# Kernel optimization log

Hardware: AMD Instinct MI355X
Metric: run time of the kernel (lower is better)

The kernel has to match this reference:

```python
import jax, jax.numpy as jnp
import numpy as np

B, L, E = 2, 8192, 1024
H, D = 16, 64          # num_heads, head_dim (E = H*D)
C = 256                # chunk_size
EPS = 1e-6
LN_EPS = 1e-5


def setup_inputs() -> dict:
    key = jax.random.key(0)
    ks = jax.random.split(key, 12)
    w = lambda k, shape: (jax.random.normal(k, shape, jnp.float32) * 0.02)
    return {
        "x": jax.random.normal(ks[0], (B, L, E), jnp.float32),
        "Wq": w(ks[1], (E, E)), "bq": jnp.zeros((E,), jnp.float32),
        "Wk": w(ks[2], (E, E)), "bk": jnp.zeros((E,), jnp.float32),
        "Wv": w(ks[3], (E, E)), "bv": jnp.zeros((E,), jnp.float32),
        "Wo": w(ks[4], (E, E)), "bo": jnp.zeros((E,), jnp.float32),
        "gamma": jnp.ones((E,), jnp.float32),
        "beta": jnp.zeros((E,), jnp.float32),
    }


def _split_heads(t):
    # [B, L, E] -> [B, H, L, D]
    return t.reshape(B, L, H, D).transpose(0, 2, 1, 3)


def _phi(x):
    # feature map: elu(x) + 1  (strictly positive)
    return jax.nn.elu(x) + 1.0


def _chunkwise_linear_attention(q, k, v):
    """Causal linear attention via chunkwise parallel scan.

    q, k, v: [B, H, L, D] (q, k already feature-mapped, positive).
    out[t] = q_t @ S_t / (q_t . z_t), S_t = sum_{s<=t} k_s v_s^T, z_t = sum_{s<=t} k_s.
    """
    N = L // C
    # [N, B, H, C, D]
    qc = q.reshape(B, H, N, C, D).transpose(2, 0, 1, 3, 4)
    kc = k.reshape(B, H, N, C, D).transpose(2, 0, 1, 3, 4)
    vc = v.reshape(B, H, N, C, D).transpose(2, 0, 1, 3, 4)
    mask = jnp.tril(jnp.ones((C, C), q.dtype))  # causal within chunk (inclusive)

    def step(carry, inp):
        S, z = carry                      # S: [B,H,D,D], z: [B,H,D]
        qi, ki, vi = inp                  # [B,H,C,D]
        scores = jnp.einsum("bhcd,bhed->bhce", qi, ki) * mask  # [B,H,C,C]
        num = jnp.einsum("bhcd,bhde->bhce", qi, S) \
            + jnp.einsum("bhce,bhed->bhcd", scores, vi)
        den = jnp.einsum("bhcd,bhd->bhc", qi, z) + scores.sum(-1)
        out = num / (den + EPS)[..., None]
        S = S + jnp.einsum("bhcd,bhce->bhde", ki, vi)
        z = z + ki.sum(axis=2)
        return (S, z), out

    S0 = jnp.zeros((B, H, D, D), q.dtype)
    z0 = jnp.zeros((B, H, D), q.dtype)
    _, outs = jax.lax.scan(step, (S0, z0), (qc, kc, vc))
    # [N,B,H,C,D] -> [B,H,L,D]
    return outs.transpose(1, 2, 0, 3, 4).reshape(B, H, L, D)


def _layer_norm(x, gamma, beta):
    mu = x.mean(-1, keepdims=True)
    var = ((x - mu) ** 2).mean(-1, keepdims=True)
    return gamma * (x - mu) * jax.lax.rsqrt(var + LN_EPS) + beta


def reference(x, Wq, bq, Wk, bk, Wv, bv, Wo, bo, gamma, beta):
    residual = x
    q = _phi(_split_heads(x @ Wq + bq))
    k = _phi(_split_heads(x @ Wk + bk))
    v = _split_heads(x @ Wv + bv)
    out = _chunkwise_linear_attention(q, k, v)      # [B,H,L,D]
    out = out.transpose(0, 2, 1, 3).reshape(B, L, E)
    out = out @ Wo + bo
    return _layer_norm(out + residual, gamma, beta)
```

## Files before the change

kernel.cpp:

```cpp
#include <hip/hip_runtime.h>
#include <stdint.h>

typedef __attribute__((ext_vector_type(8))) short bf16x8;
typedef __attribute__((ext_vector_type(4))) float f32x4;
typedef __attribute__((ext_vector_type(2))) unsigned int u32x2;
typedef unsigned short u16;
typedef unsigned int u32;

#define MFMA16(a, b, c) __builtin_amdgcn_mfma_f32_16x16x32_bf16((a), (b), (c), 0, 0, 0)
#define SBAR() __builtin_amdgcn_s_barrier()
#define WAITV(N) asm volatile("s_waitcnt vmcnt(" #N ")")

__device__ __forceinline__ u16 f2bf(float f) {
  union { float f; u32 u; } c; c.f = f;
  u32 u = c.u;
  return (u16)((u + 0x7FFFu + ((u >> 16) & 1u)) >> 16);
}

__device__ __forceinline__ float bf2f(u16 h) {
  union { u32 u; float f; } c;
  c.u = ((u32)h) << 16;
  return c.f;
}

__device__ __forceinline__ void gll16(const void* g, void* l) {
  __builtin_amdgcn_global_load_lds((__attribute__((address_space(1))) void*)(g),
                                   (__attribute__((address_space(3))) void*)(l),
                                   16, 0, 0);
}

__global__ __launch_bounds__(256) void cast_k(const float* __restrict__ x, u16* __restrict__ xb) {
  int idx = blockIdx.x * 256 + threadIdx.x;
#pragma unroll
  for (int it = 0; it < 4; it++) {
    size_t i = (size_t)idx + (size_t)it * 1048576;
    float4 v = ((const float4*)x)[i];
    u32x2 p;
    p.x = (u32)f2bf(v.x) | ((u32)f2bf(v.y) << 16);
    p.y = (u32)f2bf(v.z) | ((u32)f2bf(v.w) << 16);
    ((u32x2*)xb)[i] = p;
  }
}

__global__ __launch_bounds__(256) void wT_k(const float* __restrict__ Wq, const float* __restrict__ Wk,
                                            const float* __restrict__ Wv, const float* __restrict__ Wo,
                                            u16* __restrict__ wqkvT, u16* __restrict__ woT) {
  __shared__ float t[32][33];
  int which = blockIdx.z;
  const float* W = (which == 0) ? Wq : (which == 1) ? Wk : (which == 2) ? Wv : Wo;
  int k0 = blockIdx.y * 32, n0 = blockIdx.x * 32;
  int c = threadIdx.x & 31, r8 = threadIdx.x >> 5;
#pragma unroll
  for (int rr = 0; rr < 32; rr += 8)
    t[r8 + rr][c] = W[(size_t)(k0 + r8 + rr) * 1024 + n0 + c];
  __syncthreads();
  u16* outp = (which < 3) ? (wqkvT + (size_t)which * 1048576) : woT;
#pragma unroll
  for (int rr = 0; rr < 32; rr += 8)
    outp[(size_t)(n0 + r8 + rr) * 1024 + k0 + c] = f2bf(t[c][r8 + rr]);
}

__device__ __forceinline__ void stage_half(const u16* g, u16* l, int tid) {
  gll16(g, l + tid * 8);
  gll16(g + 65536, l + 4096 + tid * 8);
}

__device__ __forceinline__ bf16x8 fragld(const u16* h, int r, int slot) {
  return *(const bf16x8*)(h + r * 64 + ((slot ^ (r & 7)) << 3));
}

template <int MODE>
__global__ __launch_bounds__(512, 2) void gemm_k(
    const u16* __restrict__ A, const u16* __restrict__ Bt,
    const float* __restrict__ b0, const float* __restrict__ b1, const float* __restrict__ b2,
    u16* __restrict__ q_o, u16* __restrict__ k_o, u16* __restrict__ vt_o,
    const u16* __restrict__ xres, u16* __restrict__ y_o) {
  __shared__ u16 As[2][2][8192];
  __shared__ u16 Bs[2][2][8192];
  const int tid = threadIdx.x;
  const int wave = tid >> 6, lane = tid & 63;
  const int quad = lane >> 4, l16 = lane & 15;
  const int wr = wave >> 2, wc = wave & 3;
  const int bm = blockIdx.x, bn = blockIdx.y;
  const size_t arow = (size_t)bm * 256;
  const size_t brow = (size_t)bn * 256;

  const int r0 = tid >> 3;
  const int s8 = tid & 7;
  const int swz = (s8 ^ (r0 & 7)) << 3;
  const u16* gA = A + (arow + r0) * 1024 + swz;
  const u16* gB = Bt + (brow + r0) * 1024 + swz;

  f32x4 zero = {0.f, 0.f, 0.f, 0.f};
  f32x4 acc[8][4];
#pragma unroll
  for (int i = 0; i < 8; i++)
#pragma unroll
    for (int j = 0; j < 4; j++) acc[i][j] = zero;

  stage_half(gA, &As[0][0][0], tid);
  stage_half(gA + 131072, &As[0][1][0], tid);
  stage_half(gB, &Bs[0][0][0], tid);
  stage_half(gB + 131072, &Bs[0][1][0], tid);
  stage_half(gB + 64, &Bs[1][0][0], tid);
  stage_half(gB + 131072 + 64, &Bs[1][1][0], tid);
  WAITV(4);
  SBAR();

  const int bno = (wc & 1) * 64;
#pragma unroll 2
  for (int t = 0; t < 16; ++t) {
    const int cb = t & 1, nb = cb ^ 1;
    const u16* Ah = &As[cb][wr][0];
    const u16* Bh = &Bs[cb][wc >> 1][0];

    bf16x8 bfr[4][2];
#pragma unroll
    for (int n = 0; n < 4; n++)
#pragma unroll
      for (int ks = 0; ks < 2; ks++)
        bfr[n][ks] = fragld(Bh, bno + n * 16 + l16, ks * 4 + quad);

    {
      bf16x8 am[2][2];
#pragma unroll
      for (int m = 0; m < 2; m++)
#pragma unroll
        for (int ks = 0; ks < 2; ks++)
          am[m][ks] = fragld(Ah, m * 16 + l16, ks * 4 + quad);
      if (t < 15) stage_half(gA + (t + 1) * 64, &As[nb][0][0], tid);
      __builtin_amdgcn_s_setprio(1);
#pragma unroll
      for (int ks = 0; ks < 2; ks++)
#pragma unroll
        for (int m = 0; m < 2; m++)
#pragma unroll
          for (int n = 0; n < 4; n++) acc[m][n] = MFMA16(am[m][ks], bfr[n][ks], acc[m][n]);
      __builtin_amdgcn_s_setprio(0);
    }
    {
      bf16x8 am[2][2];
#pragma unroll
      for (int m = 0; m < 2; m++)
#pragma unroll
        for (int ks = 0; ks < 2; ks++)
          am[m][ks] = fragld(Ah, 32 + m * 16 + l16, ks * 4 + quad);
      if (t < 15) stage_half(gA + 131072 + (t + 1) * 64, &As[nb][1][0], tid);
      __builtin_amdgcn_s_setprio(1);
#pragma unroll
      for (int ks = 0; ks < 2; ks++)
#pragma unroll
        for (int m = 0; m < 2; m++)
#pragma unroll
          for (int n = 0; n < 4; n++) acc[2 + m][n] = MFMA16(am[m][ks], bfr[n][ks], acc[2 + m][n]);
      __builtin_amdgcn_s_setprio(0);
    }

    SBAR();
    __builtin_amdgcn_sched_barrier(0);

    {
      bf16x8 am[2][2];
#pragma unroll
      for (int m = 0; m < 2; m++)
#pragma unroll
        for (int ks = 0; ks < 2; ks++)
          am[m][ks] = fragld(Ah, 64 + m * 16 + l16, ks * 4 + quad);
      if (t < 14) stage_half(gB + (t + 2) * 64, &Bs[cb][0][0], tid);
      __builtin_amdgcn_s_setprio(1);
#pragma unroll
      for (int ks = 0; ks < 2; ks++)
#pragma unroll
        for (int m = 0; m < 2; m++)
#pragma unroll
          for (int n = 0; n < 4; n++) acc[4 + m][n] = MFMA16(am[m][ks], bfr[n][ks], acc[4 + m][n]);
      __builtin_amdgcn_s_setprio(0);
    }
    {
      bf16x8 am[2][2];
#pragma unroll
      for (int m = 0; m < 2; m++)
#pragma unroll
        for (int ks = 0; ks < 2; ks++)
          am[m][ks] = fragld(Ah, 96 + m * 16 + l16, ks * 4 + quad);
      if (t < 14) stage_half(gB + 131072 + (t + 2) * 64, &Bs[cb][1][0], tid);
      __builtin_amdgcn_s_setprio(1);
#pragma unroll
      for (int ks = 0; ks < 2; ks++)
#pragma unroll
        for (int m = 0; m < 2; m++)
#pragma unroll
          for (int n = 0; n < 4; n++) acc[6 + m][n] = MFMA16(am[m][ks], bfr[n][ks], acc[6 + m][n]);
      __builtin_amdgcn_s_setprio(0);
    }

    if (t < 14) {
      WAITV(4);
    } else if (t == 14) {
      WAITV(0);
    }
    SBAR();
  }

  if (MODE == 0) {
#pragma unroll
    for (int i = 0; i < 8; i++) {
      const int m0 = bm * 256 + wr * 128 + i * 16 + quad * 4;
      const int b = m0 >> 13, l0 = m0 & 8191;
      const int nch = l0 >> 8, c0 = l0 & 255;
#pragma unroll
      for (int j = 0; j < 4; j++) {
        const int n_g = bn * 256 + wc * 64 + j * 16 + l16;
        const int sec = n_g >> 10, e = n_g & 1023;
        const float* bias = (sec == 0) ? b0 : ((sec == 1) ? b1 : b2);
        const float be = bias[e];
        float v4[4];
#pragma unroll
        for (int r = 0; r < 4; r++) {
          float v = acc[i][j][r] + be;
          if (sec < 2) v = (v > 0.f) ? (v + 1.f) : __expf(v);
          v4[r] = v;
        }
        const int h = e >> 6, d = e & 63;
        const int bh = b * 16 + h;
        if (sec == 2) {
          u32x2 p;
          p.x = (u32)f2bf(v4[0]) | ((u32)f2bf(v4[1]) << 16);
          p.y = (u32)f2bf(v4[2]) | ((u32)f2bf(v4[3]) << 16);
          *(u32x2*)&vt_o[(((size_t)(bh * 32 + nch)) * 64 + d) * 256 + c0] = p;
        } else {
          u16* dst = (sec == 0) ? q_o : k_o;
          const size_t tb = (((size_t)bh * 8192 + l0) << 6) + d;
#pragma unroll
          for (int r = 0; r < 4; r++) dst[tb + (size_t)r * 64] = f2bf(v4[r]);
        }
      }
    }
  } else {
#pragma unroll
    for (int i = 0; i < 8; i++) {
#pragma unroll
      for (int j = 0; j < 4; j++) {
#pragma unroll
        for (int r = 0; r < 4; r++) {
          int m_g = bm * 256 + wr * 128 + i * 16 + quad * 4 + r;
          int n_g = bn * 256 + wc * 64 + j * 16 + l16;
          float v = acc[i][j][r] + b0[n_g] + bf2f(xres[(size_t)m_g * 1024 + n_g]);
          y_o[(size_t)m_g * 1024 + n_g] = f2bf(v);
        }
      }
    }
  }
}

__global__ __launch_bounds__(256, 2) void phaseA_k(const u16* __restrict__ kb, const u16* __restrict__ vt,
                                                   float* __restrict__ ST, float* __restrict__ zc) {
  __shared__ u16 kT[64 * 264];
  const int tid = threadIdx.x;
  const int wave = tid >> 6, lane = tid & 63;
  const int quad = lane >> 4, l16 = lane & 15;
  const int wr = wave >> 1, wc = wave & 1;
  const int bhn = blockIdx.x;
  const u16* kc = kb + (size_t)bhn * 16384;
  const u16* vtc = vt + (size_t)bhn * 16384;

#pragma unroll
  for (int t = 0; t < 2; t++) {
    const int dblk = wave + 4 * t;
#pragma unroll
    for (int itc = 0; itc < 4; itc++) {
      const int c = itc * 64 + lane;
      bf16x8 kv = *(const bf16x8*)&kc[c * 64 + dblk * 8];
#pragma unroll
      for (int j = 0; j < 8; j++) kT[(dblk * 8 + j) * 264 + c] = (u16)kv[j];
    }
  }
  __syncthreads();

  f32x4 zero = {0.f, 0.f, 0.f, 0.f};
  f32x4 t4[2][2];
  f32x4 za[2];
#pragma unroll
  for (int i = 0; i < 2; i++) {
    za[i] = zero;
#pragma unroll
    for (int j = 0; j < 2; j++) t4[i][j] = zero;
  }
  bf16x8 ones;
#pragma unroll
  for (int j = 0; j < 8; j++) ones[j] = (short)0x3F80;

#pragma unroll
  for (int ks = 0; ks < 8; ks++) {
    bf16x8 av[2], bk2[2];
#pragma unroll
    for (int t = 0; t < 2; t++) av[t] = *(const bf16x8*)&vtc[(wr * 32 + t * 16 + l16) * 256 + ks * 32 + quad * 8];
#pragma unroll
    for (int t = 0; t < 2; t++) bk2[t] = *(const bf16x8*)&kT[(wc * 32 + t * 16 + l16) * 264 + ks * 32 + quad * 8];
#pragma unroll
    for (int i = 0; i < 2; i++)
#pragma unroll
      for (int j = 0; j < 2; j++) t4[i][j] = MFMA16(av[i], bk2[j], t4[i][j]);
    if (wr == 0) {
#pragma unroll
      for (int j = 0; j < 2; j++) za[j] = MFMA16(ones, bk2[j], za[j]);
    }
  }
  float* Sg = ST + (size_t)bhn * 4096;
#pragma unroll
  for (int i = 0; i < 2; i++)
#pragma unroll
    for (int j = 0; j < 2; j++)
#pragma unroll
      for (int r = 0; r < 4; r++)
        Sg[(wr * 32 + i * 16 + quad * 4 + r) * 64 + wc * 32 + j * 16 + l16] = t4[i][j][r];
  if (wr == 0 && quad == 0) {
#pragma unroll
    for (int j = 0; j < 2; j++) zc[(size_t)bhn * 64 + wc * 32 + j * 16 + l16] = za[j][0];
  }
}

__global__ __launch_bounds__(256) void phaseB_k(const float* __restrict__ ST, const float* __restrict__ zc,
                                                u16* __restrict__ STp, u16* __restrict__ zp) {
  const int blk = blockIdx.x, tid = threadIdx.x;
  if (blk < 512) {
    const int bh = blk >> 4;
    const int e = ((blk & 15) << 8) + tid;
    const size_t base = (size_t)bh * 32 * 4096 + e;
    float run = 0.f;
#pragma unroll
    for (int n = 0; n < 32; n++) {
      float v = ST[base + (size_t)n * 4096];
      STp[base + (size_t)n * 4096] = f2bf(run);
      run += v;
    }
  } else {
    const int idx = (blk - 512) * 256 + tid;
    const int bh = idx >> 6, d = idx & 63;
    const size_t zb = (size_t)bh * 2048 + d;
    float run = 0.f;
#pragma unroll
    for (int n = 0; n < 32; n++) {
      float v = zc[zb + n * 64];
      zp[zb + n * 64] = f2bf(run);
      run += v;
    }
  }
}

__global__ __launch_bounds__(256, 2) void phaseC_k(const u16* __restrict__ qb, const u16* __restrict__ kb,
                                                   const u16* __restrict__ vt, const u16* __restrict__ STp,
                                                   const u16* __restrict__ zp, u16* __restrict__ ao) {
  __shared__ u16 P[4][64 * 72];
  const int tid = threadIdx.x;
  const int wave = tid >> 6, lane = tid & 63;
  const int quad = lane >> 4, l16 = lane & 15;
  const int bhn = blockIdx.x;
  const int bh = bhn >> 5, n = bhn & 31;
  const int b = bh >> 4, h = bh & 15;
  const size_t cbase = (size_t)bhn * 16384;
  const u16* qc = qb + cbase;
  const u16* kc = kb + cbase;
  const u16* vtc = vt + cbase;
  const u16* STg = STp + (size_t)bhn * 4096;
  const u16* zg = zp + (size_t)bhn * 64;

  f32x4 zero = {0.f, 0.f, 0.f, 0.f};
  f32x4 num[4][4];
  f32x4 den[4];
#pragma unroll
  for (int i = 0; i < 4; i++) {
    den[i] = zero;
#pragma unroll
    for (int j = 0; j < 4; j++) num[i][j] = zero;
  }
  bf16x8 ones;
#pragma unroll
  for (int j = 0; j < 8; j++) ones[j] = (short)0x3F80;

  bf16x8 aq[4][2];
#pragma unroll
  for (int i = 0; i < 4; i++)
#pragma unroll
    for (int ks = 0; ks < 2; ks++)
      aq[i][ks] = *(const bf16x8*)&qc[(wave * 64 + i * 16 + l16) * 64 + ks * 32 + quad * 8];

#pragma unroll
  for (int ks = 0; ks < 2; ks++) {
    bf16x8 bz = *(const bf16x8*)&zg[ks * 32 + quad * 8];
    bf16x8 bs[4];
#pragma unroll
    for (int j = 0; j < 4; j++) bs[j] = *(const bf16x8*)&STg[(j * 16 + l16) * 64 + ks * 32 + quad * 8];
#pragma unroll
    for (int i = 0; i < 4; i++) {
      den[i] = MFMA16(aq[i][ks], bz, den[i]);
#pragma unroll
      for (int j = 0; j < 4; j++) num[i][j] = MFMA16(aq[i][ks], bs[j], num[i][j]);
    }
  }

  u16* Pw = &P[wave][0];

  for (int cc = 0; cc <= wave; cc++) {
    bf16x8 bkf[2][4];
#pragma unroll
    for (int ks = 0; ks < 2; ks++)
#pragma unroll
      for (int j = 0; j < 4; j++)
        bkf[ks][j] = *(const bf16x8*)&kc[(cc * 64 + j * 16 + l16) * 64 + ks * 32 + quad * 8];
#pragma unroll
    for (int i = 0; i < 4; i++) {
      f32x4 sc4[4];
#pragma unroll
      for (int j = 0; j < 4; j++) sc4[j] = zero;
#pragma unroll
      for (int ks = 0; ks < 2; ks++)
#pragma unroll
        for (int j = 0; j < 4; j++) sc4[j] = MFMA16(aq[i][ks], bkf[ks][j], sc4[j]);
#pragma unroll
      for (int j = 0; j < 4; j++) {
#pragma unroll
        for (int r = 0; r < 4; r++) {
          int row = wave * 64 + i * 16 + quad * 4 + r;
          int col = cc * 64 + j * 16 + l16;
          float v = (col <= row) ? sc4[j][r] : 0.f;
          Pw[(i * 16 + quad * 4 + r) * 72 + j * 16 + l16] = f2bf(v);
        }
      }
    }
    bf16x8 bvf[2][4];
#pragma unroll
    for (int ks2 = 0; ks2 < 2; ks2++)
#pragma unroll
      for (int j = 0; j < 4; j++)
        bvf[ks2][j] = *(const bf16x8*)&vtc[(j * 16 + l16) * 256 + cc * 64 + ks2 * 32 + quad * 8];
#pragma unroll
    for (int i = 0; i < 4; i++) {
#pragma unroll
      for (int ks2 = 0; ks2 < 2; ks2++) {
        bf16x8 ap = *(const bf16x8*)&Pw[(i * 16 + l16) * 72 + ks2 * 32 + quad * 8];
#pragma unroll
        for (int j = 0; j < 4; j++) num[i][j] = MFMA16(ap, bvf[ks2][j], num[i][j]);
        den[i] = MFMA16(ap, ones, den[i]);
      }
    }
  }

#pragma unroll
  for (int i = 0; i < 4; i++)
#pragma unroll
    for (int j = 0; j < 4; j++)
#pragma unroll
      for (int r = 0; r < 4; r++) {
        int row = wave * 64 + i * 16 + quad * 4 + r;
        int col = j * 16 + l16;
        float o = num[i][j][r] / (den[i][r] + 1e-6f);
        int l = n * 256 + row;
        ao[(((size_t)b * 8192 + l) * 16 + h) * 64 + col] = f2bf(o);
      }
}

__global__ __launch_bounds__(256) void ln_k(const u16* __restrict__ y, const float* __restrict__ gamma,
                                            const float* __restrict__ beta, float* __restrict__ o) {
  int row = blockIdx.x, tid = threadIdx.x;
  u32x2 pv = ((const u32x2*)(y + (size_t)row * 1024))[tid];
  float vx = bf2f((u16)(pv.x & 0xFFFF)), vy = bf2f((u16)(pv.x >> 16));
  float vz = bf2f((u16)(pv.y & 0xFFFF)), vw = bf2f((u16)(pv.y >> 16));
  float s = vx + vy + vz + vw;
  float s2 = vx * vx + vy * vy + vz * vz + vw * vw;
#pragma unroll
  for (int off = 32; off; off >>= 1) {
    s += __shfl_down(s, off, 64);
    s2 += __shfl_down(s2, off, 64);
  }
  __shared__ float red[8];
  int wave = tid >> 6, lane = tid & 63;
  if (lane == 0) { red[wave] = s; red[4 + wave] = s2; }
  __syncthreads();
  s = red[0] + red[1] + red[2] + red[3];
  s2 = red[4] + red[5] + red[6] + red[7];
  float mu = s * 0.0009765625f;
  float var = s2 * 0.0009765625f - mu * mu;
  float inv = rsqrtf(var + 1e-5f);
  float4 g = ((const float4*)gamma)[tid];
  float4 bb = ((const float4*)beta)[tid];
  float4 ov;
  ov.x = g.x * (vx - mu) * inv + bb.x;
  ov.y = g.y * (vy - mu) * inv + bb.y;
  ov.z = g.z * (vz - mu) * inv + bb.z;
  ov.w = g.w * (vw - mu) * inv + bb.w;
  ((float4*)(o + (size_t)row * 1024))[tid] = ov;
}

extern "C" void kernel_launch(void* const* d_in, const int* in_sizes, int n_in,
                              void* d_out, int out_size, void* d_ws, size_t ws_size,
                              hipStream_t stream) {
  const float* x = (const float*)d_in[0];
  const float* Wq = (const float*)d_in[1];
  const float* bq = (const float*)d_in[2];
  const float* Wk = (const float*)d_in[3];
  const float* bk = (const float*)d_in[4];
  const float* Wv = (const float*)d_in[5];
  const float* bv = (const float*)d_in[6];
  const float* Wo = (const float*)d_in[7];
  const float* bo = (const float*)d_in[8];
  const float* gamma = (const float*)d_in[9];
  const float* beta = (const float*)d_in[10];

  char* ws = (char*)d_ws;
  u16* xb = (u16*)(ws + 0);
  u16* qb = (u16*)(ws + 33554432);
  u16* kb = (u16*)(ws + 67108864);
  u16* attno = (u16*)(ws + 100663296);
  u16* vt = (u16*)(ws + 134217728);
  u16* wqkvT = (u16*)(ws + 167772160);
  u16* woT = (u16*)(ws + 174063616);
  float* SchT = (float*)(ws + 176160768);
  float* zch = (float*)(ws + 192937984);
  u16* STp = (u16*)(ws + 193200128);
  u16* zp = (u16*)(ws + 201588736);
  u16* ypre = qb;

  cast_k<<<4096, 256, 0, stream>>>(x, xb);
  wT_k<<<dim3(32, 32, 4), 256, 0, stream>>>(Wq, Wk, Wv, Wo, wqkvT, woT);
  gemm_k<0><<<dim3(64, 12), 512, 0, stream>>>(xb, wqkvT, bq, bk, bv, qb, kb, vt, nullptr, nullptr);
  phaseA_k<<<1024, 256, 0, stream>>>(kb, vt, SchT, zch);
  phaseB_k<<<520, 256, 0, stream>>>(SchT, zch, STp, zp);
  phaseC_k<<<1024, 256, 0, stream>>>(qb, kb, vt, STp, zp, attno);
  gemm_k<1><<<dim3(64, 4), 512, 0, stream>>>(attno, woT, bo, nullptr, nullptr, nullptr, nullptr, nullptr, xb,
                                             ypre);
  ln_k<<<16384, 256, 0, stream>>>(ypre, gamma, beta, (float*)d_out);
}
```

Baseline: 360.9 us.

## Software-pipeline A-fragment LDS loads one MFMA block ahead in GEMM loop

Restructures the GEMM main loop so each quarter's A fragments are loaded from LDS while the previous quarter's MFMAs run, carrying fragments across quarters and across iterations through register double-buffering. Both A-half global stages are issued together early in the iteration, and the barriers are moved to match the new schedule. The goal is to hide LDS read latency behind matrix-core work. The cost is extra VGPR pressure from the carried fragments and an added barrier per iteration, which could lower occupancy or add stalls.

```diff
diff --git a/kernel.cpp b/kernel.cpp
--- a/kernel.cpp
+++ b/kernel.cpp
@@ -108,64 +108,59 @@
   SBAR();
 
   const int bno = (wc & 1) * 64;
+
+  bf16x8 amC[2][2];
+#pragma unroll
+  for (int m = 0; m < 2; m++)
+#pragma unroll
+    for (int ks = 0; ks < 2; ks++) amC[m][ks] = fragld(&As[0][wr][0], m * 16 + l16, ks * 4 + quad);
+
 #pragma unroll 2
   for (int t = 0; t < 16; ++t) {
     const int cb = t & 1, nb = cb ^ 1;
     const u16* Ah = &As[cb][wr][0];
     const u16* Bh = &Bs[cb][wc >> 1][0];
 
+    SBAR();
+
     bf16x8 bfr[4][2];
 #pragma unroll
     for (int n = 0; n < 4; n++)
 #pragma unroll
       for (int ks = 0; ks < 2; ks++)
         bfr[n][ks] = fragld(Bh, bno + n * 16 + l16, ks * 4 + quad);
-
     {
-      bf16x8 am[2][2];
-#pragma unroll
-      for (int m = 0; m < 2; m++)
-#pragma unroll
-        for (int ks = 0; ks < 2; ks++)
-          am[m][ks] = fragld(Ah, m * 16 + l16, ks * 4 + quad);
-      if (t < 15) stage_half(gA + (t + 1) * 64, &As[nb][0][0], tid);
+      bf16x8 amN[2][2];
+#pragma unroll
+      for (int m = 0; m < 2; m++)
+#pragma unroll
+        for (int ks = 0; ks < 2; ks++) amN[m][ks] = fragld(Ah, 32 + m * 16 + l16, ks * 4 + quad);
+      if (t < 15) {
+        stage_half(gA + (t + 1) * 64, &As[nb][0][0], tid);
+        stage_half(gA + 131072 + (t + 1) * 64, &As[nb][1][0], tid);
+      }
       __builtin_amdgcn_s_setprio(1);
 #pragma unroll
       for (int ks = 0; ks < 2; ks++)
 #pragma unroll
         for (int m = 0; m < 2; m++)
 #pragma unroll
-          for (int n = 0; n < 4; n++) acc[m][n] = MFMA16(am[m][ks], bfr[n][ks], acc[m][n]);
+          for (int n = 0; n < 4; n++) acc[m][n] = MFMA16(amC[m][ks], bfr[n][ks], acc[m][n]);
       __builtin_amdgcn_s_setprio(0);
-    }
+#pragma unroll
+      for (int m = 0; m < 2; m++)
+#pragma unroll
+        for (int ks = 0; ks < 2; ks++) amC[m][ks] = amN[m][ks];
+    }
+
+    SBAR();
+
     {
-      bf16x8 am[2][2];
-#pragma unroll
-      for (int m = 0; m < 2; m++)
-#pragma unroll
-        for (int ks = 0; ks < 2; ks++)
-          am[m][ks] = fragld(Ah, 32 + m * 16 + l16, ks * 4 + quad);
-      if (t < 15) stage_half(gA + 131072 + (t + 1) * 64, &As[nb][1][0], tid);
-      __builtin_amdgcn_s_setprio(1);
-#pragma unroll
-      for (int ks = 0; ks < 2; ks++)
-#pragma unroll
-        for (int m = 0; m < 2; m++)
-#pragma unroll
-          for (int n = 0; n < 4; n++) acc[2 + m][n] = MFMA16(am[m][ks], bfr[n][ks], acc[2 + m][n]);
-      __builtin_amdgcn_s_setprio(0);
-    }
-
-    SBAR();
-    __builtin_amdgcn_sched_barrier(0);
-
-    {
-      bf16x8 am[2][2];
-#pragma unroll
-      for (int m = 0; m < 2; m++)
-#pragma unroll
-        for (int ks = 0; ks < 2; ks++)
-          am[m][ks] = fragld(Ah, 64 + m * 16 + l16, ks * 4 + quad);
+      bf16x8 amN[2][2];
+#pragma unroll
+      for (int m = 0; m < 2; m++)
+#pragma unroll
+        for (int ks = 0; ks < 2; ks++) amN[m][ks] = fragld(Ah, 64 + m * 16 + l16, ks * 4 + quad);
       if (t < 14) stage_half(gB + (t + 2) * 64, &Bs[cb][0][0], tid);
       __builtin_amdgcn_s_setprio(1);
 #pragma unroll
@@ -173,16 +168,20 @@
 #pragma unroll
         for (int m = 0; m < 2; m++)
 #pragma unroll
-          for (int n = 0; n < 4; n++) acc[4 + m][n] = MFMA16(am[m][ks], bfr[n][ks], acc[4 + m][n]);
+          for (int n = 0; n < 4; n++) acc[2 + m][n] = MFMA16(amC[m][ks], bfr[n][ks], acc[2 + m][n]);
       __builtin_amdgcn_s_setprio(0);
-    }
+#pragma unroll
+      for (int m = 0; m < 2; m++)
+#pragma unroll
+        for (int ks = 0; ks < 2; ks++) amC[m][ks] = amN[m][ks];
+    }
+
     {
-      bf16x8 am[2][2];
-#pragma unroll
-      for (int m = 0; m < 2; m++)
-#pragma unroll
-        for (int ks = 0; ks < 2; ks++)
-          am[m][ks] = fragld(Ah, 96 + m * 16 + l16, ks * 4 + quad);
+      bf16x8 amN[2][2];
+#pragma unroll
+      for (int m = 0; m < 2; m++)
+#pragma unroll
+        for (int ks = 0; ks < 2; ks++) amN[m][ks] = fragld(Ah, 96 + m * 16 + l16, ks * 4 + quad);
       if (t < 14) stage_half(gB + 131072 + (t + 2) * 64, &Bs[cb][1][0], tid);
       __builtin_amdgcn_s_setprio(1);
 #pragma unroll
@@ -190,16 +189,50 @@
 #pragma unroll
         for (int m = 0; m < 2; m++)
 #pragma unroll
-          for (int n = 0; n < 4; n++) acc[6 + m][n] = MFMA16(am[m][ks], bfr[n][ks], acc[6 + m][n]);
+          for (int n = 0; n < 4; n++) acc[4 + m][n] = MFMA16(amC[m][ks], bfr[n][ks], acc[4 + m][n]);
       __builtin_amdgcn_s_setprio(0);
+#pragma unroll
+      for (int m = 0; m < 2; m++)
+#pragma unroll
+        for (int ks = 0; ks < 2; ks++) amC[m][ks] = amN[m][ks];
     }
 
     if (t < 14) {
       WAITV(4);
+      SBAR();
     } else if (t == 14) {
       WAITV(0);
-    }
-    SBAR();
+      SBAR();
+    }
+
+    if (t < 15) {
+      bf16x8 amN[2][2];
+#pragma unroll
+      for (int m = 0; m < 2; m++)
+#pragma unroll
+        for (int ks = 0; ks < 2; ks++) amN[m][ks] = fragld(&As[nb][wr][0], m * 16 + l16, ks * 4 + quad);
+      __builtin_amdgcn_s_setprio(1);
+#pragma unroll
+      for (int ks = 0; ks < 2; ks++)
+#pragma unroll
+        for (int m = 0; m < 2; m++)
+#pragma unroll
+          for (int n = 0; n < 4; n++) acc[6 + m][n] = MFMA16(amC[m][ks], bfr[n][ks], acc[6 + m][n]);
+      __builtin_amdgcn_s_setprio(0);
+#pragma unroll
+      for (int m = 0; m < 2; m++)
+#pragma unroll
+        for (int ks = 0; ks < 2; ks++) amC[m][ks] = amN[m][ks];
+    } else {
+      __builtin_amdgcn_s_setprio(1);
+#pragma unroll
+      for (int ks = 0; ks < 2; ks++)
+#pragma unroll
+        for (int m = 0; m < 2; m++)
+#pragma unroll
+          for (int n = 0; n < 4; n++) acc[6 + m][n] = MFMA16(amC[m][ks], bfr[n][ks], acc[6 + m][n]);
+      __builtin_amdgcn_s_setprio(0);
+    }
   }
 
   if (MODE == 0) {
```

After: 381.1 us. +5.6%, slower.

## Triple-buffer B tiles in the GEMM to drop the mid-iteration barrier

Applied to the files above, without the earlier changes.

The B operand's shared-memory staging grows from two buffers to three, rotated with a counter. With B tiles prefetched two steps ahead into a buffer no wave is reading, the barrier in the middle of each K iteration can go. All global-to-LDS prefetches for A and B are now issued at the top of the iteration, and the four M sub-blocks run as one unrolled loop with a single wait and barrier at the end. This raises LDS use to the full 160KB per block, which rules out co-residency, and the prefetches are no longer interleaved with the MFMA groups.

```diff
diff --git a/kernel.cpp b/kernel.cpp
--- a/kernel.cpp
+++ b/kernel.cpp
@@ -76,7 +76,7 @@
     u16* __restrict__ q_o, u16* __restrict__ k_o, u16* __restrict__ vt_o,
     const u16* __restrict__ xres, u16* __restrict__ y_o) {
   __shared__ u16 As[2][2][8192];
-  __shared__ u16 Bs[2][2][8192];
+  __shared__ u16 Bs[3][2][8192];
   const int tid = threadIdx.x;
   const int wave = tid >> 6, lane = tid & 63;
   const int quad = lane >> 4, l16 = lane & 15;
@@ -108,11 +108,21 @@
   SBAR();
 
   const int bno = (wc & 1) * 64;
-#pragma unroll 2
+  int br = 0;
   for (int t = 0; t < 16; ++t) {
     const int cb = t & 1, nb = cb ^ 1;
+    const int bw = (br >= 1) ? (br - 1) : 2;
     const u16* Ah = &As[cb][wr][0];
-    const u16* Bh = &Bs[cb][wc >> 1][0];
+    const u16* Bh = &Bs[br][wc >> 1][0];
+
+    if (t < 15) {
+      stage_half(gA + (t + 1) * 64, &As[nb][0][0], tid);
+      stage_half(gA + 131072 + (t + 1) * 64, &As[nb][1][0], tid);
+    }
+    if (t < 14) {
+      stage_half(gB + (t + 2) * 64, &Bs[bw][0][0], tid);
+      stage_half(gB + 131072 + (t + 2) * 64, &Bs[bw][1][0], tid);
+    }
 
     bf16x8 bfr[4][2];
 #pragma unroll
@@ -121,85 +131,34 @@
       for (int ks = 0; ks < 2; ks++)
         bfr[n][ks] = fragld(Bh, bno + n * 16 + l16, ks * 4 + quad);
 
-    {
+#pragma unroll
+    for (int q = 0; q < 4; q++) {
       bf16x8 am[2][2];
 #pragma unroll
       for (int m = 0; m < 2; m++)
 #pragma unroll
         for (int ks = 0; ks < 2; ks++)
-          am[m][ks] = fragld(Ah, m * 16 + l16, ks * 4 + quad);
-      if (t < 15) stage_half(gA + (t + 1) * 64, &As[nb][0][0], tid);
+          am[m][ks] = fragld(Ah, q * 32 + m * 16 + l16, ks * 4 + quad);
       __builtin_amdgcn_s_setprio(1);
 #pragma unroll
       for (int ks = 0; ks < 2; ks++)
 #pragma unroll
         for (int m = 0; m < 2; m++)
 #pragma unroll
-          for (int n = 0; n < 4; n++) acc[m][n] = MFMA16(am[m][ks], bfr[n][ks], acc[m][n]);
+          for (int n = 0; n < 4; n++)
+            acc[2 * q + m][n] = MFMA16(am[m][ks], bfr[n][ks], acc[2 * q + m][n]);
       __builtin_amdgcn_s_setprio(0);
     }
-    {
-      bf16x8 am[2][2];
-#pragma unroll
-      for (int m = 0; m < 2; m++)
-#pragma unroll
-        for (int ks = 0; ks < 2; ks++)
-          am[m][ks] = fragld(Ah, 32 + m * 16 + l16, ks * 4 + quad);
-      if (t < 15) stage_half(gA + 131072 + (t + 1) * 64, &As[nb][1][0], tid);
-      __builtin_amdgcn_s_setprio(1);
-#pragma unroll
-      for (int ks = 0; ks < 2; ks++)
-#pragma unroll
-        for (int m = 0; m < 2; m++)
-#pragma unroll
-          for (int n = 0; n < 4; n++) acc[2 + m][n] = MFMA16(am[m][ks], bfr[n][ks], acc[2 + m][n]);
-      __builtin_amdgcn_s_setprio(0);
-    }
-
-    SBAR();
-    __builtin_amdgcn_sched_barrier(0);
-
-    {
-      bf16x8 am[2][2];
-#pragma unroll
-      for (int m = 0; m < 2; m++)
-#pragma unroll
-        for (int ks = 0; ks < 2; ks++)
-          am[m][ks] = fragld(Ah, 64 + m * 16 + l16, ks * 4 + quad);
-      if (t < 14) stage_half(gB + (t + 2) * 64, &Bs[cb][0][0], tid);
-      __builtin_amdgcn_s_setprio(1);
-#pragma unroll
-      for (int ks = 0; ks < 2; ks++)
-#pragma unroll
-        for (int m = 0; m < 2; m++)
-#pragma unroll
-          for (int n = 0; n < 4; n++) acc[4 + m][n] = MFMA16(am[m][ks], bfr[n][ks], acc[4 + m][n]);
-      __builtin_amdgcn_s_setprio(0);
-    }
-    {
-      bf16x8 am[2][2];
-#pragma unroll
-      for (int m = 0; m < 2; m++)
-#pragma unroll
-        for (int ks = 0; ks < 2; ks++)
-          am[m][ks] = fragld(Ah, 96 + m * 16 + l16, ks * 4 + quad);
-      if (t < 14) stage_half(gB + 131072 + (t + 2) * 64, &Bs[cb][1][0], tid);
-      __builtin_amdgcn_s_setprio(1);
-#pragma unroll
-      for (int ks = 0; ks < 2; ks++)
-#pragma unroll
-        for (int m = 0; m < 2; m++)
-#pragma unroll
-          for (int n = 0; n < 4; n++) acc[6 + m][n] = MFMA16(am[m][ks], bfr[n][ks], acc[6 + m][n]);
-      __builtin_amdgcn_s_setprio(0);
-    }
-
-    if (t < 14) {
-      WAITV(4);
-    } else if (t == 14) {
-      WAITV(0);
-    }
-    SBAR();
+
+    if (t < 15) {
+      if (t < 14) {
+        WAITV(4);
+      } else {
+        WAITV(0);
+      }
+      SBAR();
+    }
+    br = (br == 2) ? 0 : br + 1;
   }
 
   if (MODE == 0) {
```

After: 385.1 us. +6.7%, slower.
